# Kernel optimization log

Measured on AMD Instinct MI355X. Metric: run time of the kernel, lower is better.

Reference implementation:

```python
import jax, jax.numpy as jnp
import numpy as np

B, S, HID = 2, 2048, 2048
H, D = 16, 128
BASE = 10000.0
NEG = -1e9


def _rope_tables(seq_len, dim, dtype):
    inv_freq = 1.0 / (BASE ** (jnp.arange(0, dim, 2, dtype=jnp.float32) / dim))
    pos = jnp.arange(seq_len, dtype=jnp.float32)
    freqs = jnp.einsum('s,d->sd', pos, inv_freq)          # [S, D/2]
    emb = jnp.concatenate([freqs, freqs], axis=-1)        # [S, D]
    return jnp.cos(emb).astype(dtype), jnp.sin(emb).astype(dtype)


def _rotate_half(x):
    x1, x2 = jnp.split(x, 2, axis=-1)
    return jnp.concatenate([-x2, x1], axis=-1)


def setup_inputs() -> dict:
    key = jax.random.key(0)
    k1, k2, k3 = jax.random.split(key, 3)
    x = jax.random.normal(k1, (B, S, HID), dtype=jnp.float32)
    w_qkv = jax.random.normal(k2, (HID, 3 * HID), dtype=jnp.float32) * (HID ** -0.5)
    w_out = jax.random.normal(k3, (HID, HID), dtype=jnp.float32) * (HID ** -0.5)
    return {"x": x, "w_qkv": w_qkv, "w_out": w_out}


def reference(x, w_qkv, w_out):
    b, s, _ = x.shape
    qkv = x @ w_qkv                                        # [B, S, 3*HID]
    qkv = qkv.reshape(b, s, 3, H, D).transpose(2, 0, 3, 1, 4)  # [3, B, H, S, D]
    q, k, v = qkv[0], qkv[1], qkv[2]
    cos, sin = _rope_tables(s, D, x.dtype)                 # [S, D]
    cos = cos[None, None]
    sin = sin[None, None]
    q = q * cos + _rotate_half(q) * sin
    k = k * cos + _rotate_half(k) * sin
    scale = 1.0 / np.sqrt(D)
    scores = jnp.einsum('bhqd,bhkd->bhqk', q, k) * scale   # [B, H, S, S]
    causal = jnp.triu(jnp.ones((s, s), dtype=bool), k=1)
    scores = jnp.where(causal[None, None], NEG, scores)
    attn = jax.nn.softmax(scores, axis=-1)
    out = jnp.einsum('bhqk,bhkd->bhqd', attn, v)           # [B, H, S, D]
    out = out.transpose(0, 2, 1, 3).reshape(b, s, H * D)
    return out @ w_out
```

## Files before the change

kernel.cpp:

```cpp
#include <hip/hip_runtime.h>
#include <hip/hip_bf16.h>

#define S_LEN 2048
#define HID_DIM 2048
#define NH 16
#define HD 128
#define N3 6144

typedef __bf16 bf16x8 __attribute__((ext_vector_type(8)));
typedef float f32x4 __attribute__((ext_vector_type(4)));
typedef float f32x16 __attribute__((ext_vector_type(16)));

#define MFMA16(a, b, c) __builtin_amdgcn_mfma_f32_16x16x32_bf16(a, b, c, 0, 0, 0)
#define MFMA32(a, b, c) __builtin_amdgcn_mfma_f32_32x32x16_bf16(a, b, c, 0, 0, 0)

__device__ __forceinline__ unsigned short f2bf(float f) {
  union { float f; unsigned u; } v; v.f = f;
  return (unsigned short)((v.u + 0x7fffu + ((v.u >> 16) & 1u)) >> 16);
}
__device__ __forceinline__ float bf2f(unsigned short h) {
  union { unsigned u; float f; } v; v.u = ((unsigned)h) << 16; return v.f;
}
__device__ __forceinline__ unsigned packbf2(float lo, float hi) {
  union { __hip_bfloat162 h2; unsigned u; } cv;
  cv.h2 = __float22bfloat162_rn(make_float2(lo, hi));
  return cv.u;
}
__device__ __forceinline__ void store_c(float* p, float v) { *p = v; }
__device__ __forceinline__ void store_c(unsigned short* p, float v) { *p = f2bf(v); }

__device__ __forceinline__ void async16(const void* g, void* l) {
  __builtin_amdgcn_global_load_lds((const __attribute__((address_space(1))) unsigned int*)g,
                                   (__attribute__((address_space(3))) unsigned int*)l,
                                   16, 0, 0);
}

template <int N> __device__ __forceinline__ void vmcnt();
template <> __device__ __forceinline__ void vmcnt<0>() { asm volatile("s_waitcnt vmcnt(0)" ::: "memory"); }
template <> __device__ __forceinline__ void vmcnt<5>() { asm volatile("s_waitcnt vmcnt(5)" ::: "memory"); }
template <> __device__ __forceinline__ void vmcnt<6>() { asm volatile("s_waitcnt vmcnt(6)" ::: "memory"); }

#define PLSWAP(a, b) asm volatile("v_permlane32_swap_b32 %0, %1" : "+v"(a), "+v"(b))

__global__ __launch_bounds__(256) void cast_bf16(const float4* __restrict__ src,
                                                 ushort4* __restrict__ dst) {
  int i = blockIdx.x * 256 + threadIdx.x;
  float4 v = src[i];
  ushort4 o;
  o.x = f2bf(v.x); o.y = f2bf(v.y); o.z = f2bf(v.z); o.w = f2bf(v.w);
  dst[i] = o;
}

__global__ __launch_bounds__(256) void transpose_cast(const float* __restrict__ src,
                                                      unsigned short* __restrict__ dst,
                                                      int R, int Ccols) {
  __shared__ float t[32][33];
  int ct = Ccols >> 5;
  int bx = blockIdx.x % ct, by = blockIdx.x / ct;
  int c0 = bx << 5, r0 = by << 5;
  int lx = threadIdx.x & 31, ly = threadIdx.x >> 5;
#pragma unroll
  for (int i = 0; i < 32; i += 8)
    t[ly + i][lx] = src[(long long)(r0 + ly + i) * Ccols + c0 + lx];
  __syncthreads();
#pragma unroll
  for (int i = 0; i < 32; i += 8)
    dst[(long long)(c0 + ly + i) * R + r0 + lx] = f2bf(t[lx][ly + i]);
}

__global__ __launch_bounds__(256) void rope_tables(float* __restrict__ cosT,
                                                   float* __restrict__ sinT) {
  int idx = blockIdx.x * 256 + threadIdx.x;
  int s = idx >> 6, i = idx & 63;
  float invf = powf(10000.0f, -(float)i * (1.0f / 64.0f));
  float a = (float)s * invf;
  cosT[idx] = cosf(a);
  sinT[idx] = sinf(a);
}

__global__ __launch_bounds__(512) void gemm256(const unsigned short* __restrict__ A,
                                               const unsigned short* __restrict__ Bt,
                                               unsigned short* __restrict__ C,
                                               int Mdim, int Ncols, int ldc, int Kdim) {
  constexpr int AEL = 256 * 64, BUFE = 2 * AEL;
  __shared__ unsigned short smem[2 * BUFE];

  const int ntn = Ncols >> 8;
  const int nwg = (Mdim >> 8) * ntn;
  int bid = blockIdx.x;
  bid = (bid & 7) * (nwg >> 3) + (bid >> 3);
  const int tm = (bid / ntn) << 8;
  const int tn = (bid % ntn) << 8;

  const int tid = threadIdx.x;
  const int w = tid >> 6, l = tid & 63;
  const int g = l >> 4, cc = l & 15;
  const int wm = w >> 2, wn = w & 3;

  const int srow = tid >> 3;
  const int schunk = (tid & 7) ^ (srow & 7);
  const unsigned short* gA = A + (long long)(tm + srow) * Kdim + schunk * 8;
  const unsigned short* gB = Bt + (long long)(tn + srow) * Kdim + schunk * 8;

  const int ch0 = ((g) ^ (cc & 7)) << 3;
  const int ch1 = ((4 + g) ^ (cc & 7)) << 3;

  f32x4 acc[8][4] = {};
  bf16x8 a[4][2], b[4][2];
  const int nk = Kdim >> 6;

#define ST_A(kt2, BUF, s) \
  async16(gA + (long long)(s) * 64 * Kdim + ((long long)(kt2) << 6), \
          smem + (BUF) * BUFE + (s) * 4096 + w * 512)
#define ST_B(kt2, BUF, s) \
  async16(gB + (long long)(s) * 64 * Kdim + ((long long)(kt2) << 6), \
          smem + (BUF) * BUFE + AEL + (s) * 4096 + w * 512)

#pragma unroll
  for (int s = 0; s < 4; ++s) ST_A(0, 0, s);
#pragma unroll
  for (int s = 0; s < 4; ++s) ST_B(0, 0, s);
  ST_A(1, 1, 0); ST_A(1, 1, 2);
  ST_B(1, 1, 0); ST_B(1, 1, 1); ST_B(1, 1, 2); ST_B(1, 1, 3);
  vmcnt<6>();
  __builtin_amdgcn_s_barrier();

#define KSTEP(kt, BUF, OBUF)                                                      \
  {                                                                               \
    const unsigned short* Ab = smem + (BUF) * BUFE + wm * (128 * 64);             \
    const unsigned short* Bb = smem + (BUF) * BUFE + AEL + wn * (64 * 64);        \
                    \
    _Pragma("unroll") for (int i = 0; i < 4; ++i) {                               \
      const int r = (i * 16 + cc) << 6;                                           \
      a[i][0] = *(const bf16x8*)(Ab + r + ch0);                                   \
      a[i][1] = *(const bf16x8*)(Ab + r + ch1);                                   \
    }                                                                             \
    _Pragma("unroll") for (int j = 0; j < 2; ++j) {                               \
      const int r = (j * 16 + cc) << 6;                                           \
      b[j][0] = *(const bf16x8*)(Bb + r + ch0);                                   \
      b[j][1] = *(const bf16x8*)(Bb + r + ch1);                                   \
    }                                                                             \
    if ((kt) + 1 < nk) { ST_A((kt) + 1, OBUF, 1); ST_A((kt) + 1, OBUF, 3); }      \
    __builtin_amdgcn_s_barrier();                                                 \
    __builtin_amdgcn_s_setprio(1);                                                \
    _Pragma("unroll") for (int i = 0; i < 4; ++i)                                 \
      _Pragma("unroll") for (int j = 0; j < 2; ++j) {                             \
        acc[i][j] = MFMA16(a[i][0], b[j][0], acc[i][j]);                          \
        acc[i][j] = MFMA16(a[i][1], b[j][1], acc[i][j]);                          \
      }                                                                           \
    __builtin_amdgcn_s_setprio(0);                                                \
    __builtin_amdgcn_s_barrier();                                                 \
                                              \
    _Pragma("unroll") for (int j = 0; j < 2; ++j) {                               \
      const int r = ((2 + j) * 16 + cc) << 6;                                     \
      b[2 + j][0] = *(const bf16x8*)(Bb + r + ch0);                               \
      b[2 + j][1] = *(const bf16x8*)(Bb + r + ch1);                               \
    }                                                                             \
    if ((kt) + 2 < nk) { ST_A((kt) + 2, BUF, 0); ST_A((kt) + 2, BUF, 2); }        \
    __builtin_amdgcn_s_barrier();                                                 \
    __builtin_amdgcn_s_setprio(1);                                                \
    _Pragma("unroll") for (int i = 0; i < 4; ++i)                                 \
      _Pragma("unroll") for (int j = 0; j < 2; ++j) {                             \
        acc[i][2 + j] = MFMA16(a[i][0], b[2 + j][0], acc[i][2 + j]);              \
        acc[i][2 + j] = MFMA16(a[i][1], b[2 + j][1], acc[i][2 + j]);              \
      }                                                                           \
    __builtin_amdgcn_s_setprio(0);                                                \
    __builtin_amdgcn_s_barrier();                                                 \
                                              \
    _Pragma("unroll") for (int i = 0; i < 4; ++i) {                               \
      const int r = ((64 + i * 16 + cc) << 6);                                    \
      a[i][0] = *(const bf16x8*)(Ab + r + ch0);                                   \
      a[i][1] = *(const bf16x8*)(Ab + r + ch1);                                   \
    }                                                                             \
    if ((kt) + 2 < nk) { ST_B((kt) + 2, BUF, 0); ST_B((kt) + 2, BUF, 1); }        \
    __builtin_amdgcn_s_barrier();                                                 \
    __builtin_amdgcn_s_setprio(1);                                                \
    _Pragma("unroll") for (int i = 0; i < 4; ++i)                                 \
      _Pragma("unroll") for (int j = 0; j < 2; ++j) {                             \
        acc[4 + i][j] = MFMA16(a[i][0], b[j][0], acc[4 + i][j]);                  \
        acc[4 + i][j] = MFMA16(a[i][1], b[j][1], acc[4 + i][j]);                  \
      }                                                                           \
    __builtin_amdgcn_s_setprio(0);                                                \
    __builtin_amdgcn_s_barrier();                                                 \
                            \
    if ((kt) + 2 < nk) { ST_B((kt) + 2, BUF, 2); ST_B((kt) + 2, BUF, 3); }        \
    __builtin_amdgcn_s_barrier();                                                 \
    __builtin_amdgcn_s_setprio(1);                                                \
    _Pragma("unroll") for (int i = 0; i < 4; ++i)                                 \
      _Pragma("unroll") for (int j = 0; j < 2; ++j) {                             \
        acc[4 + i][2 + j] = MFMA16(a[i][0], b[2 + j][0], acc[4 + i][2 + j]);      \
        acc[4 + i][2 + j] = MFMA16(a[i][1], b[2 + j][1], acc[4 + i][2 + j]);      \
      }                                                                           \
    __builtin_amdgcn_s_setprio(0);                                                \
    if ((kt) + 2 < nk) vmcnt<6>(); else vmcnt<0>();                               \
    __builtin_amdgcn_s_barrier();                                                 \
  }

  for (int kt = 0; kt < nk; kt += 2) {
    KSTEP(kt, 0, 1);
    KSTEP(kt + 1, 1, 0);
  }
#undef KSTEP
#undef ST_A
#undef ST_B

  const int crow0 = tm + wm * 128;
  const int ccol0 = tn + wn * 64;
#pragma unroll
  for (int i = 0; i < 8; ++i)
#pragma unroll
    for (int j = 0; j < 4; ++j)
#pragma unroll
      for (int p = 0; p < 4; ++p) {
        int row = crow0 + i * 16 + (g << 2) + p;
        int col = ccol0 + j * 16 + cc;
        store_c(&C[(long long)row * ldc + col], acc[i][j][p]);
      }
}

template <int BM, int BN, typename OutT>
__global__ __launch_bounds__(512) void gemm_pipe8(const unsigned short* __restrict__ A,
                                                  const unsigned short* __restrict__ Bt,
                                                  OutT* __restrict__ C,
                                                  int Mdim, int Ncols, int ldc, int Kdim) {
  constexpr int WTM = BM / 2, WTN = BN / 4;
  constexpr int MREP = WTM / 16, NREP = WTN / 16;
  constexpr int AEL = BM * 64, BEL = BN * 64, BUFE = AEL + BEL;
  constexpr int AINST = BM / 64, BINST = BN / 64;
  constexpr int AHALF = BM / 128, BHALF = BN / 128;
  constexpr int VN = BN / 64 + BM / 128;
  __shared__ unsigned short smem[2 * BUFE];

  const int ntn = Ncols / BN;
  const int nwg = (Mdim / BM) * ntn;
  int bid = blockIdx.x;
  bid = (bid & 7) * (nwg >> 3) + (bid >> 3);
  const int tm = (bid / ntn) * BM;
  const int tn = (bid % ntn) * BN;

  const int tid = threadIdx.x;
  const int w = tid >> 6, l = tid & 63;
  const int g = l >> 4, cc = l & 15;
  const int wm = w >> 2, wn = w & 3;

  const int srow = tid >> 3;
  const int schunk = (tid & 7) ^ (srow & 7);
  const unsigned short* gA = A + (long long)(tm + srow) * Kdim + schunk * 8;
  const unsigned short* gB = Bt + (long long)(tn + srow) * Kdim + schunk * 8;

  const int ch0 = ((g) ^ (cc & 7)) << 3;
  const int ch1 = ((4 + g) ^ (cc & 7)) << 3;

  f32x4 acc[MREP][NREP] = {};
  bf16x8 a[MREP / 2][2], b[NREP][2];

  const int nk = Kdim >> 6;

#define STAGE_A(kt2, s) \
  async16(gA + (long long)(s) * 64 * Kdim + ((long long)(kt2) << 6), \
          smem + ((kt2) & 1) * BUFE + (s) * 4096 + w * 512)
#define STAGE_B(kt2, s) \
  async16(gB + (long long)(s) * 64 * Kdim + ((long long)(kt2) << 6), \
          smem + ((kt2) & 1) * BUFE + AEL + (s) * 4096 + w * 512)

#pragma unroll
  for (int s = 0; s < AINST; ++s) STAGE_A(0, s);
#pragma unroll
  for (int s = 0; s < BINST; ++s) STAGE_B(0, s);
#pragma unroll
  for (int s = 0; s < BINST; ++s) STAGE_B(1, s);
#pragma unroll
  for (int s = 0; s < AHALF; ++s) STAGE_A(1, s);
  vmcnt<VN>();
  __builtin_amdgcn_s_barrier();

  for (int kt = 0; kt < nk; ++kt) {
    const int buf = kt & 1;
    const unsigned short* Ab = smem + buf * BUFE + (wm * WTM) * 64;
    const unsigned short* Bb = smem + buf * BUFE + AEL + (wn * WTN) * 64;

#pragma unroll
    for (int i = 0; i < MREP / 2; ++i) {
      const int r = (i * 16 + cc) << 6;
      a[i][0] = *(const bf16x8*)(Ab + r + ch0);
      a[i][1] = *(const bf16x8*)(Ab + r + ch1);
    }
#pragma unroll
    for (int j = 0; j < NREP; ++j) {
      const int r = (j * 16 + cc) << 6;
      b[j][0] = *(const bf16x8*)(Bb + r + ch0);
      b[j][1] = *(const bf16x8*)(Bb + r + ch1);
    }
    if (kt + 1 < nk) {
#pragma unroll
      for (int s = AHALF; s < AINST; ++s) STAGE_A(kt + 1, s);
    }
    __builtin_amdgcn_s_barrier();
    __builtin_amdgcn_s_setprio(1);
#pragma unroll
    for (int i = 0; i < MREP / 2; ++i)
#pragma unroll
      for (int j = 0; j < NREP / 2; ++j) {
        acc[i][j] = MFMA16(a[i][0], b[j][0], acc[i][j]);
        acc[i][j] = MFMA16(a[i][1], b[j][1], acc[i][j]);
      }
    __builtin_amdgcn_s_setprio(0);
    __builtin_amdgcn_s_barrier();

    if (kt + 2 < nk) {
#pragma unroll
      for (int s = 0; s < BHALF; ++s) STAGE_B(kt + 2, s);
    }
    __builtin_amdgcn_s_barrier();
    __builtin_amdgcn_s_setprio(1);
#pragma unroll
    for (int i = 0; i < MREP / 2; ++i)
#pragma unroll
      for (int j = 0; j < NREP / 2; ++j) {
        f32x4& ac = acc[i][NREP / 2 + j];
        ac = MFMA16(a[i][0], b[NREP / 2 + j][0], ac);
        ac = MFMA16(a[i][1], b[NREP / 2 + j][1], ac);
      }
    __builtin_amdgcn_s_setprio(0);
    __builtin_amdgcn_s_barrier();

#pragma unroll
    for (int i = 0; i < MREP / 2; ++i) {
      const int r = ((WTM / 2) + i * 16 + cc) << 6;
      a[i][0] = *(const bf16x8*)(Ab + r + ch0);
      a[i][1] = *(const bf16x8*)(Ab + r + ch1);
    }
    if (kt + 2 < nk) {
#pragma unroll
      for (int s = BHALF; s < BINST; ++s) STAGE_B(kt + 2, s);
    }
    __builtin_amdgcn_s_barrier();
    __builtin_amdgcn_s_setprio(1);
#pragma unroll
    for (int i = 0; i < MREP / 2; ++i)
#pragma unroll
      for (int j = 0; j < NREP / 2; ++j) {
        f32x4& ac = acc[MREP / 2 + i][j];
        ac = MFMA16(a[i][0], b[j][0], ac);
        ac = MFMA16(a[i][1], b[j][1], ac);
      }
    __builtin_amdgcn_s_setprio(0);
    __builtin_amdgcn_s_barrier();

    if (kt + 2 < nk) {
#pragma unroll
      for (int s = 0; s < AHALF; ++s) STAGE_A(kt + 2, s);
    }
    __builtin_amdgcn_s_barrier();
    __builtin_amdgcn_s_setprio(1);
#pragma unroll
    for (int i = 0; i < MREP / 2; ++i)
#pragma unroll
      for (int j = 0; j < NREP / 2; ++j) {
        f32x4& ac = acc[MREP / 2 + i][NREP / 2 + j];
        ac = MFMA16(a[i][0], b[NREP / 2 + j][0], ac);
        ac = MFMA16(a[i][1], b[NREP / 2 + j][1], ac);
      }
    __builtin_amdgcn_s_setprio(0);
    if (kt + 2 < nk) vmcnt<VN>(); else vmcnt<0>();
    __builtin_amdgcn_s_barrier();
  }
#undef STAGE_A
#undef STAGE_B

  const int crow0 = tm + wm * WTM;
  const int ccol0 = tn + wn * WTN;
#pragma unroll
  for (int i = 0; i < MREP; ++i)
#pragma unroll
    for (int j = 0; j < NREP; ++j)
#pragma unroll
      for (int p = 0; p < 4; ++p) {
        int row = crow0 + i * 16 + (g << 2) + p;
        int col = ccol0 + j * 16 + cc;
        store_c(&C[(long long)row * ldc + col], acc[i][j][p]);
      }
}

__global__ __launch_bounds__(256) void split_rope(const unsigned short* __restrict__ qkv,
                                                  const float* __restrict__ cosT,
                                                  const float* __restrict__ sinT,
                                                  unsigned short* __restrict__ Qb,
                                                  unsigned short* __restrict__ Kb,
                                                  unsigned short* __restrict__ Vt) {
  __shared__ unsigned short vtile[32][128];
  const int bid = blockIdx.x;
  const int st = bid & 63;
  const int h = (bid >> 6) & 15;
  const int b = bid >> 10;
  const int s0 = st << 5;
  const int t = threadIdx.x;
  const int d = t & 127;
  const int sl0 = t >> 7;
  const int dh = d & 63;
  const float sgn = (d < 64) ? -1.0f : 1.0f;
  const float qscale = 0.08838834764831845f;
#pragma unroll
  for (int it = 0; it < 16; ++it) {
    const int sl = sl0 + (it << 1);
    const int s = s0 + sl;
    const long long rb = ((long long)(b * S_LEN + s)) * N3 + h * HD;
    const float cv = cosT[(s << 6) + dh];
    const float sv = sinT[(s << 6) + dh];
    float qv = bf2f(qkv[rb + d]);
    float qo = bf2f(qkv[rb + (d ^ 64)]);
    float kv = bf2f(qkv[rb + HID_DIM + d]);
    float ko = bf2f(qkv[rb + HID_DIM + (d ^ 64)]);
    const long long ob = ((long long)((b * NH + h) * S_LEN + s)) * HD + d;
    Qb[ob] = f2bf((qv * cv + sgn * qo * sv) * qscale);
    Kb[ob] = f2bf(kv * cv + sgn * ko * sv);
    vtile[sl][d] = qkv[rb + 2 * HID_DIM + d];
  }
  __syncthreads();
  const int dr = t >> 1;
  const int sh = (t & 1) << 4;
  unsigned short tv[16];
#pragma unroll
  for (int j = 0; j < 16; ++j) tv[j] = vtile[sh + j][dr];
  uint4 u0, u1;
  u0.x = (unsigned)tv[0] | ((unsigned)tv[1] << 16);
  u0.y = (unsigned)tv[2] | ((unsigned)tv[3] << 16);
  u0.z = (unsigned)tv[4] | ((unsigned)tv[5] << 16);
  u0.w = (unsigned)tv[6] | ((unsigned)tv[7] << 16);
  u1.x = (unsigned)tv[8] | ((unsigned)tv[9] << 16);
  u1.y = (unsigned)tv[10] | ((unsigned)tv[11] << 16);
  u1.z = (unsigned)tv[12] | ((unsigned)tv[13] << 16);
  u1.w = (unsigned)tv[14] | ((unsigned)tv[15] << 16);
  const long long vb = ((long long)((b * NH + h) * HD + dr)) * S_LEN + s0 + sh;
  *(uint4*)(Vt + vb) = u0;
  *(uint4*)(Vt + vb + 8) = u1;
}

__global__ __launch_bounds__(256) void flash_attn(const unsigned short* __restrict__ Qg,
                                                  const unsigned short* __restrict__ Kg,
                                                  const unsigned short* __restrict__ Vt,
                                                  unsigned short* __restrict__ Ob) {
  __shared__ unsigned short smem[32768];
  const int id = blockIdx.x;
  const int bh = id & 31;
  const int qtr = (id >> 5) & 7;
  const int qt = (id >> 8) ? qtr : 15 - qtr;
  const int Q0 = qt << 7;
  const int b = bh >> 4, h = bh & 15;
  const long long base = (long long)bh * (S_LEN * HD);
  const int tid = threadIdx.x, w = tid >> 6, l = tid & 63;
  const int hi = l >> 5, q = l & 31;
  const int q0w = Q0 + (w << 5);
  const int g = l >> 4, c = l & 15;

  bf16x8 qf[8];
  {
    const unsigned short* qp = Qg + base + (long long)(q0w + q) * HD + (hi << 3);
#pragma unroll
    for (int s = 0; s < 8; ++s) qf[s] = *(const bf16x8*)(qp + (s << 4));
  }

  f32x16 oacc[4] = {};
  float m = -1e30f, lsum = 0.f;

  const int nt = (qt << 1) + 2;

  auto STAGE = [&](int kv0, int buf) {
    unsigned short* ks = smem + buf * 8192;
    unsigned short* vs = smem + 16384 + buf * 8192;
#pragma unroll
    for (int j = 0; j < 4; ++j) {
      int row = (w << 4) + (j << 2) + g;
      int chunk = c ^ (row & 7);
      async16(Kg + base + (long long)(kv0 + row) * HD + (chunk << 3),
              ks + (((w << 4) + (j << 2)) << 7));
    }
#pragma unroll
    for (int j = 0; j < 4; ++j) {
      int dr = (w << 5) + (j << 3) + (l >> 3);
      int chunk = (l & 7) ^ (dr & 7);
      async16(Vt + base + (long long)dr * S_LEN + kv0 + (chunk << 3),
              vs + (((w << 5) + (j << 3)) << 6));
    }
  };

  STAGE(0, 0);
  __syncthreads();

  int cur = 0;
  for (int t = 0; t < nt; ++t) {
    const int kv0 = t << 6;
    if (t + 1 < nt) STAGE((t + 1) << 6, cur ^ 1);

    if (kv0 < q0w + 32) {
      const unsigned short* ks = smem + cur * 8192;
      const unsigned short* vs = smem + 16384 + cur * 8192;

      f32x16 sa[2] = {};
#pragma unroll
      for (int h2 = 0; h2 < 2; ++h2) {
        const char* kb = (const char*)ks + (((h2 << 5) + q) << 8);
        const int r7 = q & 7;
#pragma unroll
        for (int s = 0; s < 8; ++s) {
          bf16x8 kf = *(const bf16x8*)(kb + ((((s << 1) + hi) ^ r7) << 4));
          sa[h2] = MFMA32(kf, qf[s], sa[h2]);
        }
      }

      if (kv0 + 63 > q0w) {
        const int qq = q0w + q;
#pragma unroll
        for (int h2 = 0; h2 < 2; ++h2)
#pragma unroll
          for (int j = 0; j < 16; ++j) {
            int kv = kv0 + (h2 << 5) + (j & 3) + ((j >> 2) << 3) + (hi << 2);
            if (kv > qq) sa[h2][j] = -1e30f;
          }
      }

      float t0 = sa[0][0], t1 = sa[0][1], t2 = sa[0][2], t3 = sa[0][3];
#pragma unroll
      for (int j = 4; j < 16; j += 4) {
        t0 = fmaxf(t0, sa[0][j]);     t1 = fmaxf(t1, sa[0][j + 1]);
        t2 = fmaxf(t2, sa[0][j + 2]); t3 = fmaxf(t3, sa[0][j + 3]);
      }
#pragma unroll
      for (int j = 0; j < 16; j += 4) {
        t0 = fmaxf(t0, sa[1][j]);     t1 = fmaxf(t1, sa[1][j + 1]);
        t2 = fmaxf(t2, sa[1][j + 2]); t3 = fmaxf(t3, sa[1][j + 3]);
      }
      float tmax = fmaxf(fmaxf(t0, t1), fmaxf(t2, t3));
      {
        float tcp;
        asm volatile("v_mov_b32 %0, %1" : "=v"(tcp) : "v"(tmax));
        PLSWAP(tmax, tcp);
        tmax = fmaxf(tmax, tcp);
      }
      float mn = fmaxf(m, tmax);
      float fsc = __expf(m - mn);
      m = mn;
      float s0 = 0.f, s1 = 0.f, s2 = 0.f, s3 = 0.f;
#pragma unroll
      for (int h2 = 0; h2 < 2; ++h2)
#pragma unroll
        for (int j = 0; j < 16; j += 4) {
          float p0 = __expf(sa[h2][j] - mn);
          float p1 = __expf(sa[h2][j + 1] - mn);
          float p2 = __expf(sa[h2][j + 2] - mn);
          float p3 = __expf(sa[h2][j + 3] - mn);
          sa[h2][j] = p0; sa[h2][j + 1] = p1;
          sa[h2][j + 2] = p2; sa[h2][j + 3] = p3;
          s0 += p0; s1 += p1; s2 += p2; s3 += p3;
        }
      float ps = (s0 + s1) + (s2 + s3);
      {
        float pcp;
        asm volatile("v_mov_b32 %0, %1" : "=v"(pcp) : "v"(ps));
        PLSWAP(ps, pcp);
        ps = ps + pcp;
      }
      lsum = lsum * fsc + ps;
#pragma unroll
      for (int db = 0; db < 4; ++db)
#pragma unroll
        for (int j = 0; j < 16; ++j) oacc[db][j] *= fsc;

      unsigned up[2][8];
#pragma unroll
      for (int h2 = 0; h2 < 2; ++h2)
#pragma unroll
        for (int k = 0; k < 8; ++k)
          up[h2][k] = packbf2(sa[h2][2 * k], sa[h2][2 * k + 1]);
      union Frag { unsigned u[4]; bf16x8 v; } pf[4];
#pragma unroll
      for (int s = 0; s < 4; ++s) {
        int h2 = s >> 1, q4 = (s & 1) << 2;
        unsigned a0 = up[h2][q4 + 0], b0 = up[h2][q4 + 2];
        unsigned a1 = up[h2][q4 + 1], b1 = up[h2][q4 + 3];
        PLSWAP(a0, b0);
        PLSWAP(a1, b1);
        pf[s].u[0] = a0; pf[s].u[1] = a1;
        pf[s].u[2] = b0; pf[s].u[3] = b1;
      }

#pragma unroll
      for (int db = 0; db < 4; ++db) {
        const char* vb = (const char*)vs + (((db << 5) + q) << 7);
        const int d7 = q & 7;
#pragma unroll
        for (int s = 0; s < 4; ++s) {
          bf16x8 vf = *(const bf16x8*)(vb + ((((s << 1) + hi) ^ d7) << 4));
          oacc[db] = MFMA32(vf, pf[s].v, oacc[db]);
        }
      }
    }

    __syncthreads();
    cur ^= 1;
  }

  const float rl = 1.0f / lsum;
#pragma unroll
  for (int db = 0; db < 4; ++db)
#pragma unroll
    for (int jg = 0; jg < 4; ++jg) {
      int d = (db << 5) + (jg << 3) + (hi << 2);
      unsigned v0 = packbf2(oacc[db][4 * jg] * rl, oacc[db][4 * jg + 1] * rl);
      unsigned v1 = packbf2(oacc[db][4 * jg + 2] * rl, oacc[db][4 * jg + 3] * rl);
      *(uint2*)(smem + (((w << 5) + q) << 7) + d) = make_uint2(v0, v1);
    }
  __syncthreads();
  {
    const int qr = tid >> 1;
    const int dh = (tid & 1) << 6;
    const uint4* src = (const uint4*)(smem + (qr << 7) + dh);
    uint4* dst = (uint4*)(Ob + (long long)((b << 11) + Q0 + qr) * HID_DIM + (h << 7) + dh);
#pragma unroll
    for (int cc2 = 0; cc2 < 8; ++cc2) dst[cc2] = src[cc2];
  }
}

extern "C" void kernel_launch(void* const* d_in, const int* in_sizes, int n_in,
                              void* d_out, int out_size, void* d_ws, size_t ws_size,
                              hipStream_t stream) {
  (void)in_sizes; (void)n_in; (void)out_size; (void)ws_size;
  const float* x = (const float*)d_in[0];
  const float* w_qkv = (const float*)d_in[1];
  const float* w_out = (const float*)d_in[2];
  float* out = (float*)d_out;
  char* ws = (char*)d_ws;

  unsigned short* xb    = (unsigned short*)(ws);
  unsigned short* wqkvT = (unsigned short*)(ws + 16777216);
  unsigned short* woutT = (unsigned short*)(ws + 41943040);
  unsigned short* qkv   = (unsigned short*)(ws + 50331648);
  unsigned short* Qb    = (unsigned short*)(ws + 100663296);
  unsigned short* Kb    = (unsigned short*)(ws + 117440512);
  unsigned short* Vt    = (unsigned short*)(ws + 134217728);
  float* cosT = (float*)(ws + 150994944);
  float* sinT = (float*)(ws + 151519232);
  unsigned short* Ob = qkv;

  cast_bf16<<<8192, 256, 0, stream>>>((const float4*)x, (ushort4*)xb);
  transpose_cast<<<12288, 256, 0, stream>>>(w_qkv, wqkvT, 2048, 6144);
  transpose_cast<<<4096, 256, 0, stream>>>(w_out, woutT, 2048, 2048);
  rope_tables<<<512, 256, 0, stream>>>(cosT, sinT);
  gemm256<<<256, 512, 0, stream>>>(xb, wqkvT, qkv, 4096, 4096, 6144, 2048);
  gemm_pipe8<128, 256, unsigned short><<<256, 512, 0, stream>>>(
      xb, wqkvT + (long long)4096 * 2048, qkv + 4096, 4096, 2048, 6144, 2048);
  split_rope<<<2048, 256, 0, stream>>>(qkv, cosT, sinT, Qb, Kb, Vt);
  flash_attn<<<512, 256, 0, stream>>>(Qb, Kb, Vt, Ob);
  gemm_pipe8<128, 256, float><<<256, 512, 0, stream>>>(Ob, woutT, out, 4096, 2048, 2048, 2048);
}
```

Baseline: 273.4 us.

## Shrink flash-attention blocks to 64 query rows with single-buffered KV staging

Flash attention now runs 1024 blocks of two waves, each covering 64 query rows, instead of 512 blocks of four waves covering 128 rows. The K/V LDS staging drops from double-buffered asynchronous prefetch to a single buffer with a sync after each load, halving shared memory per block. Blocks are ordered longest causal tile first. The intent is higher occupancy and better load balance across the causal triangle. The costs are twice as many K/V tile loads in total and no overlap between global loads and MFMA work inside a block.

```diff
diff --git a/kernel.cpp b/kernel.cpp
--- a/kernel.cpp
+++ b/kernel.cpp
@@ -436,22 +436,20 @@
   *(uint4*)(Vt + vb + 8) = u1;
 }
 
-__global__ __launch_bounds__(256) void flash_attn(const unsigned short* __restrict__ Qg,
+__global__ __launch_bounds__(128) void flash_attn(const unsigned short* __restrict__ Qg,
                                                   const unsigned short* __restrict__ Kg,
                                                   const unsigned short* __restrict__ Vt,
                                                   unsigned short* __restrict__ Ob) {
-  __shared__ unsigned short smem[32768];
+  __shared__ unsigned short smem[16384];
   const int id = blockIdx.x;
   const int bh = id & 31;
-  const int qtr = (id >> 5) & 7;
-  const int qt = (id >> 8) ? qtr : 15 - qtr;
-  const int Q0 = qt << 7;
+  const int qt = 31 - (id >> 5);
+  const int Q0 = qt << 6;
   const int b = bh >> 4, h = bh & 15;
   const long long base = (long long)bh * (S_LEN * HD);
   const int tid = threadIdx.x, w = tid >> 6, l = tid & 63;
   const int hi = l >> 5, q = l & 31;
   const int q0w = Q0 + (w << 5);
-  const int g = l >> 4, c = l & 15;
 
   bf16x8 qf[8];
   {
@@ -463,141 +461,129 @@
   f32x16 oacc[4] = {};
   float m = -1e30f, lsum = 0.f;
 
-  const int nt = (qt << 1) + 2;
-
-  auto STAGE = [&](int kv0, int buf) {
-    unsigned short* ks = smem + buf * 8192;
-    unsigned short* vs = smem + 16384 + buf * 8192;
-#pragma unroll
-    for (int j = 0; j < 4; ++j) {
-      int row = (w << 4) + (j << 2) + g;
-      int chunk = c ^ (row & 7);
+  const int nt = qt + 1;
+  unsigned short* ks = smem;
+  unsigned short* vs = smem + 8192;
+
+  for (int t = 0; t < nt; ++t) {
+    const int kv0 = t << 6;
+
+#pragma unroll
+    for (int j = 0; j < 8; ++j) {
+      int row = (j << 3) + (w << 2) + (l >> 4);
+      int chunk = (l & 15) ^ (row & 7);
       async16(Kg + base + (long long)(kv0 + row) * HD + (chunk << 3),
-              ks + (((w << 4) + (j << 2)) << 7));
-    }
-#pragma unroll
-    for (int j = 0; j < 4; ++j) {
-      int dr = (w << 5) + (j << 3) + (l >> 3);
+              ks + (((j << 3) + (w << 2)) << 7));
+    }
+#pragma unroll
+    for (int j = 0; j < 8; ++j) {
+      int dr = (j << 4) + (w << 3) + (l >> 3);
       int chunk = (l & 7) ^ (dr & 7);
       async16(Vt + base + (long long)dr * S_LEN + kv0 + (chunk << 3),
-              vs + (((w << 5) + (j << 3)) << 6));
-    }
-  };
-
-  STAGE(0, 0);
-  __syncthreads();
-
-  int cur = 0;
-  for (int t = 0; t < nt; ++t) {
-    const int kv0 = t << 6;
-    if (t + 1 < nt) STAGE((t + 1) << 6, cur ^ 1);
-
-    if (kv0 < q0w + 32) {
-      const unsigned short* ks = smem + cur * 8192;
-      const unsigned short* vs = smem + 16384 + cur * 8192;
-
-      f32x16 sa[2] = {};
-#pragma unroll
-      for (int h2 = 0; h2 < 2; ++h2) {
-        const char* kb = (const char*)ks + (((h2 << 5) + q) << 8);
-        const int r7 = q & 7;
-#pragma unroll
-        for (int s = 0; s < 8; ++s) {
-          bf16x8 kf = *(const bf16x8*)(kb + ((((s << 1) + hi) ^ r7) << 4));
-          sa[h2] = MFMA32(kf, qf[s], sa[h2]);
+              vs + (((j << 4) + (w << 3)) << 6));
+    }
+    __syncthreads();
+
+    f32x16 sa[2] = {};
+#pragma unroll
+    for (int h2 = 0; h2 < 2; ++h2) {
+      const char* kb = (const char*)ks + (((h2 << 5) + q) << 8);
+      const int r7 = q & 7;
+#pragma unroll
+      for (int s = 0; s < 8; ++s) {
+        bf16x8 kf = *(const bf16x8*)(kb + ((((s << 1) + hi) ^ r7) << 4));
+        sa[h2] = MFMA32(kf, qf[s], sa[h2]);
+      }
+    }
+
+    if (kv0 + 63 > q0w) {
+      const int qq = q0w + q;
+#pragma unroll
+      for (int h2 = 0; h2 < 2; ++h2)
+#pragma unroll
+        for (int j = 0; j < 16; ++j) {
+          int kv = kv0 + (h2 << 5) + (j & 3) + ((j >> 2) << 3) + (hi << 2);
+          if (kv > qq) sa[h2][j] = -1e30f;
         }
-      }
-
-      if (kv0 + 63 > q0w) {
-        const int qq = q0w + q;
-#pragma unroll
-        for (int h2 = 0; h2 < 2; ++h2)
-#pragma unroll
-          for (int j = 0; j < 16; ++j) {
-            int kv = kv0 + (h2 << 5) + (j & 3) + ((j >> 2) << 3) + (hi << 2);
-            if (kv > qq) sa[h2][j] = -1e30f;
-          }
-      }
-
-      float t0 = sa[0][0], t1 = sa[0][1], t2 = sa[0][2], t3 = sa[0][3];
-#pragma unroll
-      for (int j = 4; j < 16; j += 4) {
-        t0 = fmaxf(t0, sa[0][j]);     t1 = fmaxf(t1, sa[0][j + 1]);
-        t2 = fmaxf(t2, sa[0][j + 2]); t3 = fmaxf(t3, sa[0][j + 3]);
-      }
+    }
+
+    float t0 = sa[0][0], t1 = sa[0][1], t2 = sa[0][2], t3 = sa[0][3];
+#pragma unroll
+    for (int j = 4; j < 16; j += 4) {
+      t0 = fmaxf(t0, sa[0][j]);     t1 = fmaxf(t1, sa[0][j + 1]);
+      t2 = fmaxf(t2, sa[0][j + 2]); t3 = fmaxf(t3, sa[0][j + 3]);
+    }
+#pragma unroll
+    for (int j = 0; j < 16; j += 4) {
+      t0 = fmaxf(t0, sa[1][j]);     t1 = fmaxf(t1, sa[1][j + 1]);
+      t2 = fmaxf(t2, sa[1][j + 2]); t3 = fmaxf(t3, sa[1][j + 3]);
+    }
+    float tmax = fmaxf(fmaxf(t0, t1), fmaxf(t2, t3));
+    {
+      float tcp;
+      asm volatile("v_mov_b32 %0, %1" : "=v"(tcp) : "v"(tmax));
+      PLSWAP(tmax, tcp);
+      tmax = fmaxf(tmax, tcp);
+    }
+    float mn = fmaxf(m, tmax);
+    float fsc = __expf(m - mn);
+    m = mn;
+    float s0 = 0.f, s1 = 0.f, s2 = 0.f, s3 = 0.f;
+#pragma unroll
+    for (int h2 = 0; h2 < 2; ++h2)
 #pragma unroll
       for (int j = 0; j < 16; j += 4) {
-        t0 = fmaxf(t0, sa[1][j]);     t1 = fmaxf(t1, sa[1][j + 1]);
-        t2 = fmaxf(t2, sa[1][j + 2]); t3 = fmaxf(t3, sa[1][j + 3]);
-      }
-      float tmax = fmaxf(fmaxf(t0, t1), fmaxf(t2, t3));
-      {
-        float tcp;
-        asm volatile("v_mov_b32 %0, %1" : "=v"(tcp) : "v"(tmax));
-        PLSWAP(tmax, tcp);
-        tmax = fmaxf(tmax, tcp);
-      }
-      float mn = fmaxf(m, tmax);
-      float fsc = __expf(m - mn);
-      m = mn;
-      float s0 = 0.f, s1 = 0.f, s2 = 0.f, s3 = 0.f;
-#pragma unroll
-      for (int h2 = 0; h2 < 2; ++h2)
-#pragma unroll
-        for (int j = 0; j < 16; j += 4) {
-          float p0 = __expf(sa[h2][j] - mn);
-          float p1 = __expf(sa[h2][j + 1] - mn);
-          float p2 = __expf(sa[h2][j + 2] - mn);
-          float p3 = __expf(sa[h2][j + 3] - mn);
-          sa[h2][j] = p0; sa[h2][j + 1] = p1;
-          sa[h2][j + 2] = p2; sa[h2][j + 3] = p3;
-          s0 += p0; s1 += p1; s2 += p2; s3 += p3;
-        }
-      float ps = (s0 + s1) + (s2 + s3);
-      {
-        float pcp;
-        asm volatile("v_mov_b32 %0, %1" : "=v"(pcp) : "v"(ps));
-        PLSWAP(ps, pcp);
-        ps = ps + pcp;
-      }
-      lsum = lsum * fsc + ps;
-#pragma unroll
-      for (int db = 0; db < 4; ++db)
-#pragma unroll
-        for (int j = 0; j < 16; ++j) oacc[db][j] *= fsc;
-
-      unsigned up[2][8];
-#pragma unroll
-      for (int h2 = 0; h2 < 2; ++h2)
-#pragma unroll
-        for (int k = 0; k < 8; ++k)
-          up[h2][k] = packbf2(sa[h2][2 * k], sa[h2][2 * k + 1]);
-      union Frag { unsigned u[4]; bf16x8 v; } pf[4];
+        float p0 = __expf(sa[h2][j] - mn);
+        float p1 = __expf(sa[h2][j + 1] - mn);
+        float p2 = __expf(sa[h2][j + 2] - mn);
+        float p3 = __expf(sa[h2][j + 3] - mn);
+        sa[h2][j] = p0; sa[h2][j + 1] = p1;
+        sa[h2][j + 2] = p2; sa[h2][j + 3] = p3;
+        s0 += p0; s1 += p1; s2 += p2; s3 += p3;
+      }
+    float ps = (s0 + s1) + (s2 + s3);
+    {
+      float pcp;
+      asm volatile("v_mov_b32 %0, %1" : "=v"(pcp) : "v"(ps));
+      PLSWAP(ps, pcp);
+      ps = ps + pcp;
+    }
+    lsum = lsum * fsc + ps;
+#pragma unroll
+    for (int db = 0; db < 4; ++db)
+#pragma unroll
+      for (int j = 0; j < 16; ++j) oacc[db][j] *= fsc;
+
+    unsigned up[2][8];
+#pragma unroll
+    for (int h2 = 0; h2 < 2; ++h2)
+#pragma unroll
+      for (int k = 0; k < 8; ++k)
+        up[h2][k] = packbf2(sa[h2][2 * k], sa[h2][2 * k + 1]);
+    union Frag { unsigned u[4]; bf16x8 v; } pf[4];
+#pragma unroll
+    for (int s = 0; s < 4; ++s) {
+      int h2 = s >> 1, q4 = (s & 1) << 2;
+      unsigned a0 = up[h2][q4 + 0], b0 = up[h2][q4 + 2];
+      unsigned a1 = up[h2][q4 + 1], b1 = up[h2][q4 + 3];
+      PLSWAP(a0, b0);
+      PLSWAP(a1, b1);
+      pf[s].u[0] = a0; pf[s].u[1] = a1;
+      pf[s].u[2] = b0; pf[s].u[3] = b1;
+    }
+
+#pragma unroll
+    for (int db = 0; db < 4; ++db) {
+      const char* vb = (const char*)vs + (((db << 5) + q) << 7);
+      const int d7 = q & 7;
 #pragma unroll
       for (int s = 0; s < 4; ++s) {
-        int h2 = s >> 1, q4 = (s & 1) << 2;
-        unsigned a0 = up[h2][q4 + 0], b0 = up[h2][q4 + 2];
-        unsigned a1 = up[h2][q4 + 1], b1 = up[h2][q4 + 3];
-        PLSWAP(a0, b0);
-        PLSWAP(a1, b1);
-        pf[s].u[0] = a0; pf[s].u[1] = a1;
-        pf[s].u[2] = b0; pf[s].u[3] = b1;
-      }
-
-#pragma unroll
-      for (int db = 0; db < 4; ++db) {
-        const char* vb = (const char*)vs + (((db << 5) + q) << 7);
-        const int d7 = q & 7;
-#pragma unroll
-        for (int s = 0; s < 4; ++s) {
-          bf16x8 vf = *(const bf16x8*)(vb + ((((s << 1) + hi) ^ d7) << 4));
-          oacc[db] = MFMA32(vf, pf[s].v, oacc[db]);
-        }
+        bf16x8 vf = *(const bf16x8*)(vb + ((((s << 1) + hi) ^ d7) << 4));
+        oacc[db] = MFMA32(vf, pf[s].v, oacc[db]);
       }
     }
 
     __syncthreads();
-    cur ^= 1;
   }
 
   const float rl = 1.0f / lsum;
@@ -650,6 +636,6 @@
   gemm_pipe8<128, 256, unsigned short><<<256, 512, 0, stream>>>(
       xb, wqkvT + (long long)4096 * 2048, qkv + 4096, 4096, 2048, 6144, 2048);
   split_rope<<<2048, 256, 0, stream>>>(qkv, cosT, sinT, Qb, Kb, Vt);
-  flash_attn<<<512, 256, 0, stream>>>(Qb, Kb, Vt, Ob);
+  flash_attn<<<1024, 128, 0, stream>>>(Qb, Kb, Vt, Ob);
   gemm_pipe8<128, 256, float><<<256, 512, 0, stream>>>(Ob, woutT, out, 4096, 2048, 2048, 2048);
 }
```

After: 281.5 us. 3.0% more time.
